# Performance work log

Measured on AMD Instinct MI355X. Metric: run time of the kernel, lower is better.

The kernel has to match this reference:

```python
import jax, jax.numpy as jnp
import numpy as np

B, T, C = 4, 2048, 2048
EPS = 1e-5


def setup_inputs() -> dict:
    key = jax.random.key(0)
    ks = jax.random.split(key, 9)
    s = 1.0 / np.sqrt(C)
    return {
        "x": jax.random.normal(ks[0], (B, T, C), jnp.float32),
        "ln_w": jnp.ones((C,), jnp.float32),
        "ln_b": jnp.zeros((C,), jnp.float32),
        "mix_k": jax.random.uniform(ks[1], (C,), jnp.float32),
        "mix_v": jax.random.uniform(ks[2], (C,), jnp.float32),
        "mix_r": jax.random.uniform(ks[3], (C,), jnp.float32),
        "time_decay": jnp.zeros((C,), jnp.float32),
        "time_first": jnp.zeros((C,), jnp.float32),
        "Wk": jax.random.normal(ks[4], (C, C), jnp.float32) * s,
        "Wv": jax.random.normal(ks[5], (C, C), jnp.float32) * s,
        "Wr": jax.random.normal(ks[6], (C, C), jnp.float32) * s,
        "Wo": jax.random.normal(ks[7], (C, C), jnp.float32) * s,
    }


def reference(x, ln_w, ln_b, mix_k, mix_v, mix_r, time_decay, time_first, Wk, Wv, Wr, Wo):
    # LayerNorm over channel dim
    mu = jnp.mean(x, axis=-1, keepdims=True)
    var = jnp.var(x, axis=-1, keepdims=True)
    xt = (x - mu) * jax.lax.rsqrt(var + EPS) * ln_w + ln_b  # [B,T,C]

    # x_prev at step t is xt at step t-1 (zeros at t=0) -> simple time shift
    prev = jnp.concatenate([jnp.zeros_like(xt[:, :1]), xt[:, :-1]], axis=1)

    # Batched projections (torch Linear: y = x @ W.T)
    k = jnp.einsum('btc,dc->btd', xt * mix_k + prev * (1.0 - mix_k), Wk)
    v = jnp.einsum('btc,dc->btd', xt * mix_v + prev * (1.0 - mix_v), Wv)
    r = jax.nn.sigmoid(jnp.einsum('btc,dc->btd', xt * mix_r + prev * (1.0 - mix_r), Wr))

    decay = jax.nn.sigmoid(time_decay)  # [C]
    first = jnp.exp(time_first)         # [C]

    # Elementwise linear recurrence: state_t = decay * state_{t-1} + k_t
    def step(state, k_t):
        state = state * decay + k_t
        return state, state

    _, states = jax.lax.scan(step, jnp.zeros((B, C), x.dtype), jnp.swapaxes(k, 0, 1))
    state = jnp.swapaxes(states, 0, 1)  # [B,T,C]

    rwkv = (state * first + k) * v
    return jnp.einsum('btc,dc->btd', r * rwkv, Wo)
```

## Files before the change

kernel.cpp:

```cpp
#include <hip/hip_runtime.h>
#include <math.h>

constexpr int B_ = 4;
constexpr int T_ = 2048;
constexpr int C_ = 2048;
constexpr int M_ = B_ * T_;
constexpr float EPS_ = 1e-5f;
constexpr int KSTEPS = C_ / 64;
constexpr int NCH = 32;
constexpr int CHL = T_ / NCH;

typedef __attribute__((ext_vector_type(8))) short short8;
typedef __attribute__((ext_vector_type(4))) float f32x4;

__device__ __forceinline__ unsigned short rne_bf16(float x) {
    unsigned u = __float_as_uint(x);
    unsigned r = u + 0x7FFFu + ((u >> 16) & 1u);
    return (unsigned short)(r >> 16);
}
__device__ __forceinline__ float bf16_to_f32(unsigned short h) {
    return __uint_as_float((unsigned)h << 16);
}

__global__ __launch_bounds__(256) void ln_mix3_kernel(
        const float* __restrict__ x,
        const float* __restrict__ w,
        const float* __restrict__ bias,
        const float* __restrict__ mxk,
        const float* __restrict__ mxv,
        const float* __restrict__ mxr,
        unsigned short* __restrict__ ak,
        unsigned short* __restrict__ av,
        unsigned short* __restrict__ ar) {
    const int m = blockIdx.x;
    const int tid = threadIdx.x;
    const bool hasPrev = (m & (T_ - 1)) != 0;
    const float* xm = x + (size_t)m * C_;

    float4 a0 = ((const float4*)xm)[tid];
    float4 a1 = ((const float4*)xm)[tid + 256];
    float4 p0 = make_float4(0.f, 0.f, 0.f, 0.f), p1 = p0;
    if (hasPrev) {
        p0 = ((const float4*)(xm - C_))[tid];
        p1 = ((const float4*)(xm - C_))[tid + 256];
    }

    float sm = a0.x + a0.y + a0.z + a0.w + a1.x + a1.y + a1.z + a1.w;
    float qm = a0.x*a0.x + a0.y*a0.y + a0.z*a0.z + a0.w*a0.w
             + a1.x*a1.x + a1.y*a1.y + a1.z*a1.z + a1.w*a1.w;
    float sp = p0.x + p0.y + p0.z + p0.w + p1.x + p1.y + p1.z + p1.w;
    float qp = p0.x*p0.x + p0.y*p0.y + p0.z*p0.z + p0.w*p0.w
             + p1.x*p1.x + p1.y*p1.y + p1.z*p1.z + p1.w*p1.w;

    #pragma unroll
    for (int off = 32; off > 0; off >>= 1) {
        sm += __shfl_down(sm, off, 64);
        qm += __shfl_down(qm, off, 64);
        sp += __shfl_down(sp, off, 64);
        qp += __shfl_down(qp, off, 64);
    }
    __shared__ float red[20];
    const int wid = tid >> 6, lane = tid & 63;
    if (lane == 0) {
        red[wid * 4 + 0] = sm; red[wid * 4 + 1] = qm;
        red[wid * 4 + 2] = sp; red[wid * 4 + 3] = qp;
    }
    __syncthreads();
    if (tid == 0) {
        float tsm = 0.f, tqm = 0.f, tsp = 0.f, tqp = 0.f;
        #pragma unroll
        for (int i = 0; i < 4; ++i) {
            tsm += red[i * 4 + 0]; tqm += red[i * 4 + 1];
            tsp += red[i * 4 + 2]; tqp += red[i * 4 + 3];
        }
        const float mum = tsm / (float)C_;
        const float varm = tqm / (float)C_ - mum * mum;
        const float mup = tsp / (float)C_;
        const float varp = tqp / (float)C_ - mup * mup;
        red[16] = mum; red[17] = rsqrtf(varm + EPS_);
        red[18] = mup; red[19] = rsqrtf(varp + EPS_);
    }
    __syncthreads();
    const float mum = red[16], rsm = red[17];
    const float mup = red[18], rsp = red[19];

    float4 w0 = ((const float4*)w)[tid];
    float4 w1 = ((const float4*)w)[tid + 256];
    float4 b0 = ((const float4*)bias)[tid];
    float4 b1 = ((const float4*)bias)[tid + 256];

    const float avv[8] = {a0.x, a0.y, a0.z, a0.w, a1.x, a1.y, a1.z, a1.w};
    const float pvv[8] = {p0.x, p0.y, p0.z, p0.w, p1.x, p1.y, p1.z, p1.w};
    const float wvv[8] = {w0.x, w0.y, w0.z, w0.w, w1.x, w1.y, w1.z, w1.w};
    const float bvv[8] = {b0.x, b0.y, b0.z, b0.w, b1.x, b1.y, b1.z, b1.w};

    float lm[8], lp[8];
    #pragma unroll
    for (int j = 0; j < 8; ++j) {
        lm[j] = (avv[j] - mum) * rsm * wvv[j] + bvv[j];
        lp[j] = hasPrev ? (pvv[j] - mup) * rsp * wvv[j] + bvv[j] : 0.f;
    }

    const size_t rowbase = (size_t)m * C_;
    auto emit = [&](const float* __restrict__ mx, unsigned short* __restrict__ hi) {
        float4 m0 = ((const float4*)mx)[tid];
        float4 m1 = ((const float4*)mx)[tid + 256];
        const float mm[8] = {m0.x, m0.y, m0.z, m0.w, m1.x, m1.y, m1.z, m1.w};
        ushort4 h[2];
        #pragma unroll
        for (int half = 0; half < 2; ++half) {
            unsigned short hh[4];
            #pragma unroll
            for (int j = 0; j < 4; ++j) {
                const int c = half * 4 + j;
                hh[j] = rne_bf16(lp[c] + (lm[c] - lp[c]) * mm[c]);
            }
            h[half].x = hh[0]; h[half].y = hh[1]; h[half].z = hh[2]; h[half].w = hh[3];
        }
        ((ushort4*)(hi + rowbase))[tid] = h[0];
        ((ushort4*)(hi + rowbase))[tid + 256] = h[1];
    };
    emit(mxk, ak);
    emit(mxv, av);
    emit(mxr, ar);
}

__global__ __launch_bounds__(256) void wconv_kernel(const float* __restrict__ W,
                                                    unsigned short* __restrict__ hi) {
    const int i = blockIdx.x * 256 + threadIdx.x;
    float4 w = ((const float4*)W)[i];
    ushort4 h;
    h.x = rne_bf16(w.x);
    h.y = rne_bf16(w.y);
    h.z = rne_bf16(w.z);
    h.w = rne_bf16(w.w);
    ((ushort4*)hi)[i] = h;
}

template <bool SIG, bool OUTBF16>
__global__ __launch_bounds__(512, 2) void gemm_mfma(const unsigned short* __restrict__ Ahi,
                                                    const unsigned short* __restrict__ Whi,
                                                    float* __restrict__ Yf,
                                                    unsigned short* __restrict__ Yh) {
    __shared__ unsigned short lds[2][2][256 * 64];

    const int tid = threadIdx.x;
    const int lane = tid & 63;
    const int wid = tid >> 6;
    const int wr = wid >> 2;
    const int wcn = wid & 3;

    const int bid = blockIdx.x;
    const int swz = (bid & 7) * 32 + (bid >> 3);
    const int m0 = (swz >> 3) * 256;
    const int n0 = (swz & 7) * 256;

    const unsigned short* gA[4];
    const unsigned short* gB[4];
    #pragma unroll
    for (int j = 0; j < 4; ++j) {
        const int ci = j * 512 + tid;
        const int r = ci >> 3, p = ci & 7;
        const int s = p ^ (r & 7);
        gA[j] = Ahi + (size_t)(m0 + r) * C_ + s * 8;
        gB[j] = Whi + (size_t)(n0 + r) * C_ + s * 8;
    }
    const int stage_off = wid * 512;

    const int fr = lane & 15;
    const int kg = lane >> 4;
    const int pS0 = (kg + 0) ^ (fr & 7);
    const int pS1 = (kg + 4) ^ (fr & 7);
    const int baseA0 = (wr * 128 + fr) * 64 + pS0 * 8;
    const int baseA1 = (wr * 128 + fr) * 64 + pS1 * 8;
    const int baseB0 = (wcn * 64 + fr) * 64 + pS0 * 8;
    const int baseB1 = (wcn * 64 + fr) * 64 + pS1 * 8;

    f32x4 acc[8][4] = {};

    auto ISSUE = [&](int buf, int t, int j) {
        const int ko = t * 64;
        __builtin_amdgcn_global_load_lds(
            (const __attribute__((address_space(1))) unsigned int*)(gA[j] + ko),
            (__attribute__((address_space(3))) unsigned int*)&lds[buf][0][j * 4096 + stage_off],
            16, 0, 0);
        __builtin_amdgcn_global_load_lds(
            (const __attribute__((address_space(1))) unsigned int*)(gB[j] + ko),
            (__attribute__((address_space(3))) unsigned int*)&lds[buf][1][j * 4096 + stage_off],
            16, 0, 0);
    };

    auto MFMA_QUAD = [&](int mi0, const short8* a0, const short8* a1,
                         const short8* b0, const short8* b1) {
        #pragma unroll
        for (int ni = 0; ni < 4; ++ni)
            #pragma unroll
            for (int q = 0; q < 4; ++q)
                acc[mi0 + q][ni] = __builtin_amdgcn_mfma_f32_16x16x32_bf16(a0[q], b0[ni], acc[mi0 + q][ni], 0, 0, 0);
        #pragma unroll
        for (int ni = 0; ni < 4; ++ni)
            #pragma unroll
            for (int q = 0; q < 4; ++q)
                acc[mi0 + q][ni] = __builtin_amdgcn_mfma_f32_16x16x32_bf16(a1[q], b1[ni], acc[mi0 + q][ni], 0, 0, 0);
    };

    #pragma unroll
    for (int j = 0; j < 4; ++j) ISSUE(0, 0, j);

    for (int t = 0; t < KSTEPS; ++t) {
        const int cur = t & 1, nxt = cur ^ 1;
        const bool last = (t == KSTEPS - 1);
        const unsigned short* LA = lds[cur][0];
        const unsigned short* LB = lds[cur][1];

        short8 b0[4], b1[4];

        if (!last) {
            ISSUE(nxt, t + 1, 0);
            ISSUE(nxt, t + 1, 1);
            asm volatile("s_waitcnt vmcnt(4)" ::: "memory");
        } else {
            asm volatile("s_waitcnt vmcnt(0)" ::: "memory");
        }
        __builtin_amdgcn_s_barrier();
        #pragma unroll
        for (int ni = 0; ni < 4; ++ni) {
            b0[ni] = *(const short8*)&LB[baseB0 + ni * 1024];
            b1[ni] = *(const short8*)&LB[baseB1 + ni * 1024];
        }
        {
            short8 a0[4], a1[4];
            #pragma unroll
            for (int q = 0; q < 4; ++q) {
                a0[q] = *(const short8*)&LA[baseA0 + q * 1024];
                a1[q] = *(const short8*)&LA[baseA1 + q * 1024];
            }
            asm volatile("s_waitcnt lgkmcnt(0)" ::: "memory");
            __builtin_amdgcn_s_setprio(1);
            MFMA_QUAD(0, a0, a1, b0, b1);
            __builtin_amdgcn_s_setprio(0);
        }
        __builtin_amdgcn_s_barrier();

        {
            short8 a0[4], a1[4];
            #pragma unroll
            for (int q = 0; q < 4; ++q) {
                a0[q] = *(const short8*)&LA[baseA0 + (4 + q) * 1024];
                a1[q] = *(const short8*)&LA[baseA1 + (4 + q) * 1024];
            }
            if (!last) {
                ISSUE(nxt, t + 1, 2);
                ISSUE(nxt, t + 1, 3);
            }
            __builtin_amdgcn_s_barrier();
            asm volatile("s_waitcnt lgkmcnt(0)" ::: "memory");
            __builtin_amdgcn_s_setprio(1);
            MFMA_QUAD(4, a0, a1, b0, b1);
            __builtin_amdgcn_s_setprio(0);
            __builtin_amdgcn_s_barrier();
        }
    }

    const int orow = m0 + wr * 128 + (lane >> 4) * 4;
    const int ocol = n0 + wcn * 64 + fr;
    #pragma unroll
    for (int mi = 0; mi < 8; ++mi)
        #pragma unroll
        for (int ni = 0; ni < 4; ++ni)
            #pragma unroll
            for (int rr = 0; rr < 4; ++rr) {
                float v = acc[mi][ni][rr];
                if (SIG) v = 1.f / (1.f + expf(-v));
                const size_t idx = (size_t)(orow + mi * 16 + rr) * C_ + ocol + ni * 16;
                if (OUTBF16) Yh[idx] = rne_bf16(v);
                else         Yf[idx] = v;
            }
}

__global__ __launch_bounds__(256) void wkv_scan1(const unsigned short* __restrict__ k,
                                                 const float* __restrict__ time_decay,
                                                 float* __restrict__ chend) {
    const int c0 = (blockIdx.x * 256 + threadIdx.x) * 2;
    const int j = blockIdx.y;
    const int b = blockIdx.z;
    const float2 td = *(const float2*)&time_decay[c0];
    const float d0 = 1.f / (1.f + expf(-td.x));
    const float d1 = 1.f / (1.f + expf(-td.y));
    size_t base = ((size_t)b * T_ + (size_t)j * CHL) * C_ + c0;
    float s0 = 0.f, s1 = 0.f;
    #pragma unroll 8
    for (int t = 0; t < CHL; ++t) {
        const ushort2 kt = *(const ushort2*)&k[base];
        s0 = s0 * d0 + bf16_to_f32(kt.x);
        s1 = s1 * d1 + bf16_to_f32(kt.y);
        base += C_;
    }
    *(float2*)&chend[((size_t)b * NCH + j) * C_ + c0] = make_float2(s0, s1);
}

__global__ __launch_bounds__(256) void wkv_scan2(const unsigned short* __restrict__ k,
                                                 const unsigned short* __restrict__ v,
                                                 const unsigned short* __restrict__ r,
                                                 const float* __restrict__ time_decay,
                                                 const float* __restrict__ time_first,
                                                 const float* __restrict__ chend,
                                                 unsigned short* __restrict__ yhi) {
    const int c0 = (blockIdx.x * 256 + threadIdx.x) * 2;
    const int j = blockIdx.y;
    const int b = blockIdx.z;
    const float2 td = *(const float2*)&time_decay[c0];
    const float2 tf = *(const float2*)&time_first[c0];
    const float d0 = 1.f / (1.f + expf(-td.x));
    const float d1 = 1.f / (1.f + expf(-td.y));
    const float f0 = expf(tf.x);
    const float f1 = expf(tf.y);

    float dL0 = d0, dL1 = d1;
    #pragma unroll
    for (int i = 0; i < 6; ++i) { dL0 *= dL0; dL1 *= dL1; }

    float s0 = 0.f, s1 = 0.f;
    for (int i = 0; i < j; ++i) {
        const float2 e = *(const float2*)&chend[((size_t)b * NCH + i) * C_ + c0];
        s0 = s0 * dL0 + e.x;
        s1 = s1 * dL1 + e.y;
    }

    size_t base = ((size_t)b * T_ + (size_t)j * CHL) * C_ + c0;
    #pragma unroll 4
    for (int t = 0; t < CHL; ++t) {
        const ushort2 kt = *(const ushort2*)&k[base];
        const ushort2 vt = *(const ushort2*)&v[base];
        const ushort2 rt = *(const ushort2*)&r[base];
        const float k0 = bf16_to_f32(kt.x), k1 = bf16_to_f32(kt.y);
        s0 = s0 * d0 + k0;
        s1 = s1 * d1 + k1;
        const float y0 = bf16_to_f32(rt.x) * ((s0 * f0 + k0) * bf16_to_f32(vt.x));
        const float y1 = bf16_to_f32(rt.y) * ((s1 * f1 + k1) * bf16_to_f32(vt.y));
        ushort2 ph; ph.x = rne_bf16(y0); ph.y = rne_bf16(y1);
        *(ushort2*)&yhi[base] = ph;
        base += C_;
    }
}

extern "C" void kernel_launch(void* const* d_in, const int* in_sizes, int n_in,
                              void* d_out, int out_size, void* d_ws, size_t ws_size,
                              hipStream_t stream) {
    const float* x          = (const float*)d_in[0];
    const float* ln_w       = (const float*)d_in[1];
    const float* ln_b       = (const float*)d_in[2];
    const float* mix_k      = (const float*)d_in[3];
    const float* mix_v      = (const float*)d_in[4];
    const float* mix_r      = (const float*)d_in[5];
    const float* time_decay = (const float*)d_in[6];
    const float* time_first = (const float*)d_in[7];
    const float* Wk         = (const float*)d_in[8];
    const float* Wv         = (const float*)d_in[9];
    const float* Wr         = (const float*)d_in[10];
    const float* Wo         = (const float*)d_in[11];
    float* out = (float*)d_out;

    const size_t planeElems = (size_t)M_ * C_;
    unsigned short* akhi = (unsigned short*)d_ws;
    unsigned short* avhi = akhi + 2 * planeElems;
    unsigned short* arhi = avhi + 2 * planeElems;
    unsigned short* whi  = arhi + 2 * planeElems;

    unsigned short* kb = arhi;
    unsigned short* vb = akhi;
    unsigned short* rb = (unsigned short*)out;
    unsigned short* yhi = avhi;
    float* chend = (float*)whi;

    const int wcBlocks = (C_ * C_ / 4) / 256;
    const dim3 wkvGrid(C_ / 512, NCH, B_);

    ln_mix3_kernel<<<M_, 256, 0, stream>>>(x, ln_w, ln_b, mix_k, mix_v, mix_r,
                                           akhi, avhi, arhi);

    wconv_kernel<<<wcBlocks, 256, 0, stream>>>(Wr, whi);
    gemm_mfma<true, true><<<256, 512, 0, stream>>>(arhi, whi, nullptr, rb);

    wconv_kernel<<<wcBlocks, 256, 0, stream>>>(Wk, whi);
    gemm_mfma<false, true><<<256, 512, 0, stream>>>(akhi, whi, nullptr, kb);

    wconv_kernel<<<wcBlocks, 256, 0, stream>>>(Wv, whi);
    gemm_mfma<false, true><<<256, 512, 0, stream>>>(avhi, whi, nullptr, vb);

    wkv_scan1<<<wkvGrid, 256, 0, stream>>>(kb, time_decay, chend);
    wkv_scan2<<<wkvGrid, 256, 0, stream>>>(kb, vb, rb, time_decay, time_first, chend,
                                           yhi);

    wconv_kernel<<<wcBlocks, 256, 0, stream>>>(Wo, whi);
    gemm_mfma<false, false><<<256, 512, 0, stream>>>(yhi, whi, out, nullptr);
}
```

Measured before the change: 361.1 us.

## Batch three projection GEMMs into one launch and fuse weight conversions

```diff
diff --git a/kernel.cpp b/kernel.cpp
--- a/kernel.cpp
+++ b/kernel.cpp
@@ -125,9 +125,23 @@
     emit(mxr, ar);
 }
 
-__global__ __launch_bounds__(256) void wconv_kernel(const float* __restrict__ W,
-                                                    unsigned short* __restrict__ hi) {
+__global__ __launch_bounds__(256) void wconv4_kernel(const float* __restrict__ W0,
+                                                     const float* __restrict__ W1,
+                                                     const float* __restrict__ W2,
+                                                     const float* __restrict__ W3,
+                                                     unsigned short* __restrict__ h0,
+                                                     unsigned short* __restrict__ h1,
+                                                     unsigned short* __restrict__ h2,
+                                                     unsigned short* __restrict__ h3) {
     const int i = blockIdx.x * 256 + threadIdx.x;
+    const float* W;
+    unsigned short* hi;
+    switch (blockIdx.y) {
+        case 0:  W = W0; hi = h0; break;
+        case 1:  W = W1; hi = h1; break;
+        case 2:  W = W2; hi = h2; break;
+        default: W = W3; hi = h3; break;
+    }
     float4 w = ((const float4*)W)[i];
     ushort4 h;
     h.x = rne_bf16(w.x);
@@ -137,11 +151,12 @@
     ((ushort4*)hi)[i] = h;
 }
 
-template <bool SIG, bool OUTBF16>
-__global__ __launch_bounds__(512, 2) void gemm_mfma(const unsigned short* __restrict__ Ahi,
-                                                    const unsigned short* __restrict__ Whi,
-                                                    float* __restrict__ Yf,
-                                                    unsigned short* __restrict__ Yh) {
+template <bool OUTBF16>
+__device__ __forceinline__ void gemm_body(const unsigned short* __restrict__ Ahi,
+                                          const unsigned short* __restrict__ Whi,
+                                          float* __restrict__ Yf,
+                                          unsigned short* __restrict__ Yh,
+                                          int bid, bool sig) {
     __shared__ unsigned short lds[2][2][256 * 64];
 
     const int tid = threadIdx.x;
@@ -150,7 +165,6 @@
     const int wr = wid >> 2;
     const int wcn = wid & 3;
 
-    const int bid = blockIdx.x;
     const int swz = (bid & 7) * 32 + (bid >> 3);
     const int m0 = (swz >> 3) * 256;
     const int n0 = (swz & 7) * 256;
@@ -271,11 +285,39 @@
             #pragma unroll
             for (int rr = 0; rr < 4; ++rr) {
                 float v = acc[mi][ni][rr];
-                if (SIG) v = 1.f / (1.f + expf(-v));
+                if (sig) v = 1.f / (1.f + expf(-v));
                 const size_t idx = (size_t)(orow + mi * 16 + rr) * C_ + ocol + ni * 16;
                 if (OUTBF16) Yh[idx] = rne_bf16(v);
                 else         Yf[idx] = v;
             }
+}
+
+__global__ __launch_bounds__(512, 2) void gemm_proj3(const unsigned short* __restrict__ ar,
+                                                     const unsigned short* __restrict__ ak,
+                                                     const unsigned short* __restrict__ av,
+                                                     const unsigned short* __restrict__ wr,
+                                                     const unsigned short* __restrict__ wk,
+                                                     const unsigned short* __restrict__ wv,
+                                                     unsigned short* __restrict__ rb,
+                                                     unsigned short* __restrict__ kb,
+                                                     unsigned short* __restrict__ vb) {
+    const int bid = blockIdx.x;
+    const int proj = bid >> 8;
+    const int inner = bid & 255;
+    const unsigned short* A;
+    const unsigned short* W;
+    unsigned short* Y;
+    bool sig;
+    if (proj == 0)      { A = ar; W = wr; Y = rb; sig = true;  }
+    else if (proj == 1) { A = ak; W = wk; Y = kb; sig = false; }
+    else                { A = av; W = wv; Y = vb; sig = false; }
+    gemm_body<true>(A, W, nullptr, Y, inner, sig);
+}
+
+__global__ __launch_bounds__(512, 2) void gemm_out(const unsigned short* __restrict__ A,
+                                                   const unsigned short* __restrict__ W,
+                                                   float* __restrict__ Y) {
+    gemm_body<false>(A, W, Y, nullptr, blockIdx.x, false);
 }
 
 __global__ __launch_bounds__(256) void wkv_scan1(const unsigned short* __restrict__ k,
@@ -361,37 +403,34 @@
     const float* Wo         = (const float*)d_in[11];
     float* out = (float*)d_out;
 
-    const size_t planeElems = (size_t)M_ * C_;
-    unsigned short* akhi = (unsigned short*)d_ws;
-    unsigned short* avhi = akhi + 2 * planeElems;
-    unsigned short* arhi = avhi + 2 * planeElems;
-    unsigned short* whi  = arhi + 2 * planeElems;
-
-    unsigned short* kb = arhi;
-    unsigned short* vb = akhi;
+    const size_t P = (size_t)M_ * C_;
+    unsigned short* ak = (unsigned short*)d_ws;
+    unsigned short* av = ak + P;
+    unsigned short* ar = av + P;
+    unsigned short* kb = ar + P;
+    unsigned short* vb = kb + P;
+    unsigned short* wr = vb + P;
+    unsigned short* wk = wr + P / 4;
+    unsigned short* wv = wk + P / 4;
+    unsigned short* wo = wv + P / 4;
+
     unsigned short* rb = (unsigned short*)out;
-    unsigned short* yhi = avhi;
-    float* chend = (float*)whi;
-
-    const int wcBlocks = (C_ * C_ / 4) / 256;
+    unsigned short* yhi = ak;
+    float* chend = (float*)wr;
+
+    const dim3 wcGrid((C_ * C_ / 4) / 256, 4);
     const dim3 wkvGrid(C_ / 512, NCH, B_);
 
+    wconv4_kernel<<<wcGrid, 256, 0, stream>>>(Wr, Wk, Wv, Wo, wr, wk, wv, wo);
+
     ln_mix3_kernel<<<M_, 256, 0, stream>>>(x, ln_w, ln_b, mix_k, mix_v, mix_r,
-                                           akhi, avhi, arhi);
-
-    wconv_kernel<<<wcBlocks, 256, 0, stream>>>(Wr, whi);
-    gemm_mfma<true, true><<<256, 512, 0, stream>>>(arhi, whi, nullptr, rb);
-
-    wconv_kernel<<<wcBlocks, 256, 0, stream>>>(Wk, whi);
-    gemm_mfma<false, true><<<256, 512, 0, stream>>>(akhi, whi, nullptr, kb);
-
-    wconv_kernel<<<wcBlocks, 256, 0, stream>>>(Wv, whi);
-    gemm_mfma<false, true><<<256, 512, 0, stream>>>(avhi, whi, nullptr, vb);
+                                           ak, av, ar);
+
+    gemm_proj3<<<768, 512, 0, stream>>>(ar, ak, av, wr, wk, wv, rb, kb, vb);
 
     wkv_scan1<<<wkvGrid, 256, 0, stream>>>(kb, time_decay, chend);
     wkv_scan2<<<wkvGrid, 256, 0, stream>>>(kb, vb, rb, time_decay, time_first, chend,
                                            yhi);
 
-    wconv_kernel<<<wcBlocks, 256, 0, stream>>>(Wo, whi);
-    gemm_mfma<false, false><<<256, 512, 0, stream>>>(yhi, whi, out, nullptr);
-}
+    gemm_out<<<256, 512, 0, stream>>>(yhi, wo, out);
+}
```

Result: no change. 354.1 us (-1.9%).
